# Performance work log

Measured on AMD Instinct MI355X. Metric: run time of the kernel, lower is better.

The kernel has to match this reference:

```python
import jax, jax.numpy as jnp
import numpy as np

B, F, S, H1, H2 = 4096, 512, 32, 64, 32


def setup_inputs() -> dict:
    key = jax.random.key(0)
    ks = jax.random.split(key, 9)
    x = jax.random.normal(ks[0], (B, F), dtype=jnp.float32)
    # ExU layer init: truncated_normal(mean=4, std=0.5) on weight, std=0.5 on bias
    W0 = 4.0 + 0.5 * jax.random.normal(ks[1], (F, S, S), dtype=jnp.float32)
    b0 = 0.5 * jax.random.normal(ks[2], (F, S), dtype=jnp.float32)
    # ReLU hidden layers: xavier-ish weights, small biases
    W1 = jax.random.normal(ks[3], (F, S, H1), dtype=jnp.float32) * np.sqrt(2.0 / (S + H1))
    b1 = 0.5 * jax.random.normal(ks[4], (F, S), dtype=jnp.float32)
    W2 = jax.random.normal(ks[5], (F, H1, H2), dtype=jnp.float32) * np.sqrt(2.0 / (H1 + H2))
    b2 = 0.5 * jax.random.normal(ks[6], (F, H1), dtype=jnp.float32)
    Wl = jax.random.normal(ks[7], (F, H2), dtype=jnp.float32) * np.sqrt(2.0 / (H2 + 1))
    out_bias = jnp.zeros((1,), dtype=jnp.float32)
    return {"x": x, "W0": W0, "b0": b0, "W1": W1, "b1": b1,
            "W2": W2, "b2": b2, "Wl": Wl, "out_bias": out_bias}


def reference(x, W0, b0, W1, b1, W2, b2, Wl, out_bias):
    # ExU shallow layer per feature: clip((x_f - b0_f) @ exp(W0_f), 0, 1)
    # x[:, :, None] - b0 broadcasts scalar feature to (B, F, S)
    h = jnp.clip(jnp.einsum('bfs,fsh->bfh', x[:, :, None] - b0[None], jnp.exp(W0)), 0.0, 1.0)
    # ReLU hidden layers: relu((h - b) @ W)
    h = jax.nn.relu(jnp.einsum('bfs,fsh->bfh', h - b1[None], W1))   # (B, F, H1)
    h = jax.nn.relu(jnp.einsum('bfh,fho->bfo', h - b2[None], W2))   # (B, F, H2)
    # per-feature Linear(H2 -> 1, no bias), concatenated over features
    f_out = jnp.einsum('bfo,fo->bf', h, Wl)                          # (B, F)
    # forward_type == 'sum' (feature_dropout is identity at inference)
    return f_out.sum(axis=-1) + out_bias[0], f_out
```

## Files before the change

kernel.cpp:

```cpp
#include <hip/hip_runtime.h>

typedef __attribute__((ext_vector_type(8))) short short8;
typedef __attribute__((ext_vector_type(4))) float f32x4;
typedef unsigned int uint32;

namespace {
constexpr int F = 512, NB = 4096;
constexpr int RB = 512;
constexpr int FPB = 4;
constexpr int NFQ = F / FPB;
constexpr size_t OFF_W1F  = 0;
constexpr size_t OFF_W2F  = OFF_W1F + (size_t)F * 4 * 64 * 16;
constexpr size_t OFF_TAB  = OFF_W2F + (size_t)F * 4 * 64 * 16;
constexpr size_t OFF_PART = OFF_TAB + (size_t)F * 160 * 4;
constexpr size_t WS_NEED  = OFF_PART + (size_t)NFQ * NB * 4;
}

__device__ __forceinline__ uint32 cvtpk(float lo, float hi) {
    uint32 r;
    asm("v_cvt_pk_bf16_f32 %0, %1, %2" : "=v"(r) : "v"(lo), "v"(hi));
    return r;
}
__device__ __forceinline__ float clip01(float v) {
    return __builtin_amdgcn_fmed3f(v, 0.f, 1.f);
}

__global__ __launch_bounds__(256) void nam_prep(
    const float* __restrict__ W0, const float* __restrict__ b0,
    const float* __restrict__ W1, const float* __restrict__ b1,
    const float* __restrict__ W2, const float* __restrict__ b2,
    char* __restrict__ ws)
{
    const int f = blockIdx.x;
    const int t = threadIdx.x;
    const int lane = t & 63, w = t >> 6, g = lane >> 4, rr = lane & 15;

    __shared__ float LW[2048];
    __shared__ float red[256], red2[256];

    const float* W0f = W0 + (size_t)f * 1024;
    const float* W1f = W1 + (size_t)f * 2048;
    const float* W2f = W2 + (size_t)f * 2048;
    float* tab = (float*)(ws + OFF_TAB) + (size_t)f * 160;
    union U8 { uint32 u[4]; short8 s8; };

    *(float4*)&LW[t * 4] = *(const float4*)&W0f[t * 4];
    __syncthreads();
    {
        int j = t & 31, sc = t >> 5;
        float a = 0.f, c = 0.f;
#pragma unroll
        for (int k = 0; k < 4; ++k) {
            int s = sc * 4 + k;
            float e = expf(LW[s * 32 + j]);
            a += e; c += b0[f * 32 + s] * e;
        }
        red[sc * 32 + j] = a; red2[sc * 32 + j] = c;
    }
    __syncthreads();
    if (t < 32) {
        float a = 0.f, c = 0.f;
#pragma unroll
        for (int k = 0; k < 8; ++k) { a += red[k * 32 + t]; c += red2[k * 32 + t]; }
        tab[t] = a; tab[32 + t] = -c;
    }
    __syncthreads();

    *(float4*)&LW[t * 4]        = *(const float4*)&W1f[t * 4];
    *(float4*)&LW[1024 + t * 4] = *(const float4*)&W1f[1024 + t * 4];
    __syncthreads();
    {
        int j = t & 63, sc = t >> 6;
        float d = 0.f;
#pragma unroll
        for (int k = 0; k < 8; ++k) {
            int s = sc * 8 + k;
            d += b1[f * 32 + s] * LW[s * 64 + j];
        }
        red[sc * 64 + j] = d;
    }
    {
        int mi = w;
        int col = 32 * (mi & 1) + 8 * (rr >> 2) + 4 * (mi >> 1) + (rr & 3);
        int base = (8 * g) * 64 + col;
        U8 v;
        v.u[0] = cvtpk(LW[base],       LW[base + 64]);
        v.u[1] = cvtpk(LW[base + 128], LW[base + 192]);
        v.u[2] = cvtpk(LW[base + 256], LW[base + 320]);
        v.u[3] = cvtpk(LW[base + 384], LW[base + 448]);
        ((short8*)(ws + OFF_W1F))[((size_t)f * 4 + mi) * 64 + lane] = v.s8;
    }
    __syncthreads();
    if (t < 64) {
        float d = red[t] + red[64 + t] + red[128 + t] + red[192 + t];
        int dst = 32 * ((t >> 2) & 1) + 16 * (t >> 5) + 4 * ((t >> 3) & 3) + (t & 3);
        tab[64 + dst] = -d;
    }
    __syncthreads();

    *(float4*)&LW[t * 4]        = *(const float4*)&W2f[t * 4];
    *(float4*)&LW[1024 + t * 4] = *(const float4*)&W2f[1024 + t * 4];
    __syncthreads();
    {
        int o = t & 31, hc = t >> 5;
        float d = 0.f;
#pragma unroll
        for (int k = 0; k < 8; ++k) {
            int h = hc * 8 + k;
            d += b2[f * 64 + h] * LW[h * 32 + o];
        }
        red[hc * 32 + o] = d;
    }
    {
        int m2 = w >> 1, kc = w & 1;
        int base = (32 * kc + 8 * g) * 32 + 16 * m2 + rr;
        U8 v;
        v.u[0] = cvtpk(LW[base],       LW[base + 32]);
        v.u[1] = cvtpk(LW[base + 64],  LW[base + 96]);
        v.u[2] = cvtpk(LW[base + 128], LW[base + 160]);
        v.u[3] = cvtpk(LW[base + 192], LW[base + 224]);
        ((short8*)(ws + OFF_W2F))[((size_t)f * 4 + m2 * 2 + kc) * 64 + lane] = v.s8;
    }
    __syncthreads();
    if (t < 32) {
        float d = 0.f;
#pragma unroll
        for (int k = 0; k < 8; ++k) d += red[k * 32 + t];
        tab[128 + t] = -d;
    }
}

__device__ __forceinline__ void tile_compute(
    float xv, const short8* w1f, const short8 (&w2f)[2][2],
    const f32x4& A0, const f32x4& A1, const f32x4& C0, const f32x4& C1,
    const f32x4* nd1, const f32x4* nd2, f32x4& c0, f32x4& c1)
{
    union U8 { uint32 u[4]; short8 s8; };
    U8 hb;
    hb.u[0] = cvtpk(clip01(fmaf(xv, A0[0], C0[0])), clip01(fmaf(xv, A0[1], C0[1])));
    hb.u[1] = cvtpk(clip01(fmaf(xv, A0[2], C0[2])), clip01(fmaf(xv, A0[3], C0[3])));
    hb.u[2] = cvtpk(clip01(fmaf(xv, A1[0], C1[0])), clip01(fmaf(xv, A1[1], C1[1])));
    hb.u[3] = cvtpk(clip01(fmaf(xv, A1[2], C1[2])), clip01(fmaf(xv, A1[3], C1[3])));
    short8 b0f = hb.s8;

    f32x4 a0 = __builtin_amdgcn_mfma_f32_16x16x32_bf16(w1f[0], b0f, nd1[0], 0, 0, 0);
    f32x4 a1 = __builtin_amdgcn_mfma_f32_16x16x32_bf16(w1f[1], b0f, nd1[1], 0, 0, 0);
    f32x4 a2 = __builtin_amdgcn_mfma_f32_16x16x32_bf16(w1f[2], b0f, nd1[2], 0, 0, 0);
    f32x4 a3 = __builtin_amdgcn_mfma_f32_16x16x32_bf16(w1f[3], b0f, nd1[3], 0, 0, 0);

    U8 r0, r1;
    r0.u[0] = cvtpk(fmaxf(a0[0], 0.f), fmaxf(a0[1], 0.f));
    r0.u[1] = cvtpk(fmaxf(a0[2], 0.f), fmaxf(a0[3], 0.f));
    r0.u[2] = cvtpk(fmaxf(a2[0], 0.f), fmaxf(a2[1], 0.f));
    r0.u[3] = cvtpk(fmaxf(a2[2], 0.f), fmaxf(a2[3], 0.f));
    r1.u[0] = cvtpk(fmaxf(a1[0], 0.f), fmaxf(a1[1], 0.f));
    r1.u[1] = cvtpk(fmaxf(a1[2], 0.f), fmaxf(a1[3], 0.f));
    r1.u[2] = cvtpk(fmaxf(a3[0], 0.f), fmaxf(a3[1], 0.f));
    r1.u[3] = cvtpk(fmaxf(a3[2], 0.f), fmaxf(a3[3], 0.f));

    c0 = __builtin_amdgcn_mfma_f32_16x16x32_bf16(w2f[0][0], r0.s8, nd2[0], 0, 0, 0);
    c0 = __builtin_amdgcn_mfma_f32_16x16x32_bf16(w2f[0][1], r1.s8, c0, 0, 0, 0);
    c1 = __builtin_amdgcn_mfma_f32_16x16x32_bf16(w2f[1][0], r0.s8, nd2[1], 0, 0, 0);
    c1 = __builtin_amdgcn_mfma_f32_16x16x32_bf16(w2f[1][1], r1.s8, c1, 0, 0, 0);
}

__global__ __launch_bounds__(256, 3) void nam_main(
    const float* __restrict__ x, const float* __restrict__ Wl,
    const char* __restrict__ ws, float* __restrict__ fout, float* __restrict__ part)
{
    const int fq = blockIdx.y;
    const int f0 = fq * FPB;
    const int rbase = blockIdx.x * RB;
    const int t = threadIdx.x;
    const int w = t >> 6, lane = t & 63;
    const int g = lane >> 4, rr = lane & 15;
    const int f = f0 + w;

    __shared__ float sx[FPB * RB];
    __shared__ float sfo[FPB * RB];

    {
        float4 v0 = *(const float4*)(x + (size_t)(rbase + t) * F + f0);
        float4 v1 = *(const float4*)(x + (size_t)(rbase + t + 256) * F + f0);
        sx[0 * RB + t] = v0.x; sx[1 * RB + t] = v0.y;
        sx[2 * RB + t] = v0.z; sx[3 * RB + t] = v0.w;
        sx[0 * RB + t + 256] = v1.x; sx[1 * RB + t + 256] = v1.y;
        sx[2 * RB + t + 256] = v1.z; sx[3 * RB + t + 256] = v1.w;
    }

    const short8* w1img = (const short8*)(ws + OFF_W1F);
    const short8* w2img = (const short8*)(ws + OFF_W2F);
    short8 w1f[4], w2f[2][2];
#pragma unroll
    for (int mi = 0; mi < 4; ++mi) w1f[mi] = w1img[((size_t)f * 4 + mi) * 64 + lane];
#pragma unroll
    for (int m2 = 0; m2 < 2; ++m2)
#pragma unroll
        for (int kc = 0; kc < 2; ++kc)
            w2f[m2][kc] = w2img[((size_t)f * 4 + m2 * 2 + kc) * 64 + lane];

    const f32x4* tabv = (const f32x4*)((const float*)(ws + OFF_TAB) + (size_t)f * 160);
    f32x4 A0 = tabv[2 * g], A1 = tabv[2 * g + 1];
    f32x4 C0 = tabv[8 + 2 * g], C1 = tabv[8 + 2 * g + 1];
    f32x4 nd1[4];
#pragma unroll
    for (int mi = 0; mi < 4; ++mi) nd1[mi] = tabv[16 + 4 * mi + g];
    f32x4 nd2[2];
#pragma unroll
    for (int m2 = 0; m2 < 2; ++m2) nd2[m2] = tabv[32 + 4 * m2 + g];
    f32x4 wl0 = *(const f32x4*)(Wl + f * 32 + 4 * g);
    f32x4 wl1 = *(const f32x4*)(Wl + f * 32 + 16 + 4 * g);

    __syncthreads();

    const float* sxf = sx + w * RB;
    float* sfof = sfo + w * RB;

    for (int k = 0; k < 16; ++k) {
        float xv0 = sxf[32 * k + rr];
        float xv1 = sxf[32 * k + 16 + rr];
        f32x4 c00, c01, c10, c11;
        tile_compute(xv0, w1f, w2f, A0, A1, C0, C1, nd1, nd2, c00, c01);
        tile_compute(xv1, w1f, w2f, A0, A1, C0, C1, nd1, nd2, c10, c11);

        float p0 = 0.f, p1 = 0.f;
#pragma unroll
        for (int r = 0; r < 4; ++r) {
            p0 = fmaf(fmaxf(c00[r], 0.f), wl0[r], p0);
            p0 = fmaf(fmaxf(c01[r], 0.f), wl1[r], p0);
            p1 = fmaf(fmaxf(c10[r], 0.f), wl0[r], p1);
            p1 = fmaf(fmaxf(c11[r], 0.f), wl1[r], p1);
        }
        p0 += __shfl_xor(p0, 16, 64);
        p0 += __shfl_xor(p0, 32, 64);
        p1 += __shfl_xor(p1, 16, 64);
        p1 += __shfl_xor(p1, 32, 64);
        if (lane < 16) {
            sfof[32 * k + lane] = p0;
            sfof[32 * k + 16 + lane] = p1;
        }
    }

    __syncthreads();

#pragma unroll
    for (int kk = 0; kk < 2; ++kk) {
        int r = t + 256 * kk;
        float v0 = sfo[0 * RB + r], v1 = sfo[1 * RB + r];
        float v2 = sfo[2 * RB + r], v3 = sfo[3 * RB + r];
        *(float4*)(fout + (size_t)(rbase + r) * F + f0) = make_float4(v0, v1, v2, v3);
        part[(size_t)fq * NB + rbase + r] = (v0 + v1) + (v2 + v3);
    }
}

__global__ __launch_bounds__(256) void nam_sum(const float* __restrict__ part,
                                               const float* __restrict__ ob,
                                               float* __restrict__ out0) {
    int r = blockIdx.x * 256 + threadIdx.x;
    float s = ob[0];
#pragma unroll 8
    for (int q = 0; q < NFQ; ++q) s += part[(size_t)q * NB + r];
    out0[r] = s;
}

namespace fbk { constexpr int S = 32, H1 = 64, H2 = 32, BLK = 256, ROWS = 2, P1 = 36; }
__global__ __launch_bounds__(256, 2) void fb_main(
    const float* __restrict__ x,  const float* __restrict__ W0,
    const float* __restrict__ b0, const float* __restrict__ W1,
    const float* __restrict__ b1, const float* __restrict__ W2,
    const float* __restrict__ b2, const float* __restrict__ Wl,
    float* __restrict__ fout) {
    using namespace fbk;
    const int f = blockIdx.y;
    const int bbase = blockIdx.x * (BLK * ROWS);
    const int t = threadIdx.x;
    __shared__ float W0e[S * S];
    __shared__ float W1t[H1 * P1];
    __shared__ float W2l[H1 * H2];
    __shared__ float sb0[S], sb1[S], sb2[H1];
    __shared__ float sA[S], sC[S], sd1[H1], sd2[H2], sWl[H2];
    {
        float4 wv = *reinterpret_cast<const float4*>(W0 + (size_t)f * S * S + t * 4);
        W0e[t * 4 + 0] = expf(wv.x); W0e[t * 4 + 1] = expf(wv.y);
        W0e[t * 4 + 2] = expf(wv.z); W0e[t * 4 + 3] = expf(wv.w);
    }
    if (t < S) sb0[t] = b0[f * S + t];
    else if (t < 2 * S) sb1[t - S] = b1[f * S + (t - S)];
    else if (t < 2 * S + H1) sb2[t - 2 * S] = b2[f * H1 + (t - 2 * S)];
    else if (t < 2 * S + H1 + H2) sWl[t - 2 * S - H1] = Wl[f * H2 + (t - 2 * S - H1)];
#pragma unroll
    for (int k = 0; k < (S * H1) / BLK; ++k) {
        int i = t + BLK * k; int s = i >> 6, j = i & 63;
        W1t[j * P1 + s] = W1[(size_t)f * S * H1 + i];
    }
#pragma unroll
    for (int k = 0; k < (H1 * H2) / BLK; ++k) {
        int i = t + BLK * k; W2l[i] = W2[(size_t)f * H1 * H2 + i];
    }
    __syncthreads();
    if (t < S) {
        int j = t; float a = 0.f, c = 0.f;
#pragma unroll
        for (int s = 0; s < S; ++s) { float e = W0e[s * S + j]; a += e; c += sb0[s] * e; }
        sA[j] = a; sC[j] = c;
    } else if (t >= 64 && t < 64 + H1) {
        int j = t - 64; float d = 0.f;
#pragma unroll
        for (int s = 0; s < S; ++s) d += sb1[s] * W1t[j * P1 + s];
        sd1[j] = d;
    } else if (t >= 128 && t < 128 + H2) {
        int o = t - 128; float d = 0.f;
#pragma unroll
        for (int h = 0; h < H1; ++h) d += sb2[h] * W2l[h * H2 + o];
        sd2[o] = d;
    }
    __syncthreads();
    const int ra = bbase + t, rb = bbase + BLK + t;
    const float xa = x[(size_t)ra * F + f], xb = x[(size_t)rb * F + f];
    float h0a[S], h0b[S];
#pragma unroll
    for (int j = 0; j < S; ++j) {
        float A = sA[j], C = sC[j];
        h0a[j] = fminf(fmaxf(fmaf(xa, A, -C), 0.f), 1.f);
        h0b[j] = fminf(fmaxf(fmaf(xb, A, -C), 0.f), 1.f);
    }
    float acc2a[H2], acc2b[H2];
#pragma unroll
    for (int o = 0; o < H2; ++o) { float d = sd2[o]; acc2a[o] = -d; acc2b[o] = -d; }
#pragma unroll 2
    for (int j = 0; j < H1; ++j) {
        float wr[S];
#pragma unroll
        for (int q = 0; q < S / 4; ++q)
            *reinterpret_cast<float4*>(&wr[4 * q]) = reinterpret_cast<const float4*>(&W1t[j * P1])[q];
        float d1j = sd1[j];
        float pa0 = -d1j, pa1 = 0.f, pb0 = -d1j, pb1 = 0.f;
#pragma unroll
        for (int s = 0; s < S; s += 2) {
            pa0 = fmaf(h0a[s], wr[s], pa0); pb0 = fmaf(h0b[s], wr[s], pb0);
            pa1 = fmaf(h0a[s + 1], wr[s + 1], pa1); pb1 = fmaf(h0b[s + 1], wr[s + 1], pb1);
        }
        float h1a = fmaxf(pa0 + pa1, 0.f), h1b = fmaxf(pb0 + pb1, 0.f);
        float w2r[H2];
#pragma unroll
        for (int q = 0; q < H2 / 4; ++q)
            *reinterpret_cast<float4*>(&w2r[4 * q]) = reinterpret_cast<const float4*>(&W2l[j * H2])[q];
#pragma unroll
        for (int o = 0; o < H2; ++o) {
            acc2a[o] = fmaf(h1a, w2r[o], acc2a[o]); acc2b[o] = fmaf(h1b, w2r[o], acc2b[o]);
        }
    }
    float outa = 0.f, outb = 0.f;
#pragma unroll
    for (int o = 0; o < H2; ++o) {
        outa = fmaf(fmaxf(acc2a[o], 0.f), sWl[o], outa);
        outb = fmaf(fmaxf(acc2b[o], 0.f), sWl[o], outb);
    }
    fout[(size_t)ra * F + f] = outa;
    fout[(size_t)rb * F + f] = outb;
}
__global__ __launch_bounds__(256) void fb_rowsum(
    const float* __restrict__ fout, const float* __restrict__ out_bias,
    float* __restrict__ out0) {
    const int wave = threadIdx.x >> 6, lane = threadIdx.x & 63;
    const int b = blockIdx.x * 4 + wave;
    float s = 0.f;
#pragma unroll
    for (int k = 0; k < F / 64; ++k) s += fout[(size_t)b * F + k * 64 + lane];
#pragma unroll
    for (int off = 32; off; off >>= 1) s += __shfl_down(s, off, 64);
    if (lane == 0) out0[b] = s + out_bias[0];
}

extern "C" void kernel_launch(void* const* d_in, const int* in_sizes, int n_in,
                              void* d_out, int out_size, void* d_ws, size_t ws_size,
                              hipStream_t stream) {
    const float* x  = (const float*)d_in[0];
    const float* W0 = (const float*)d_in[1];
    const float* b0 = (const float*)d_in[2];
    const float* W1 = (const float*)d_in[3];
    const float* b1 = (const float*)d_in[4];
    const float* W2 = (const float*)d_in[5];
    const float* b2 = (const float*)d_in[6];
    const float* Wl = (const float*)d_in[7];
    const float* ob = (const float*)d_in[8];

    float* out0 = (float*)d_out;
    float* fout = out0 + NB;

    if (ws_size >= WS_NEED) {
        char* ws = (char*)d_ws;
        float* part = (float*)(ws + OFF_PART);
        nam_prep<<<F, 256, 0, stream>>>(W0, b0, W1, b1, W2, b2, ws);
        nam_main<<<dim3(NB / RB, NFQ), 256, 0, stream>>>(x, Wl, ws, fout, part);
        nam_sum <<<NB / 256, 256, 0, stream>>>(part, ob, out0);
    } else {
        dim3 grid(NB / (fbk::BLK * fbk::ROWS), F);
        fb_main<<<grid, fbk::BLK, 0, stream>>>(x, W0, b0, W1, b1, W2, b2, Wl, fout);
        fb_rowsum<<<NB / 4, 256, 0, stream>>>(fout, ob, out0);
    }
}
```

Before: 48.90 us.

## Halve row block, process one tile per iteration, reduce partials through LDS

Halves the rows per block to 256 and raises the launch-bounds occupancy hint from 3 to 4 blocks per CU, doubling the grid. The inner loop now handles one 16-row tile per iteration instead of two. The cross-lane shuffle reduction is replaced by storing per-group partials to a shared buffer and summing them with vector LDS reads, and the x staging buffer is reused to hold per-feature outputs. The aim is lower register pressure and fewer shuffles. The cost is less ILP per wave, more LDS traffic, and weights reloaded by twice as many blocks.

```diff
diff --git a/kernel.cpp b/kernel.cpp
--- a/kernel.cpp
+++ b/kernel.cpp
@@ -6,7 +6,7 @@
 
 namespace {
 constexpr int F = 512, NB = 4096;
-constexpr int RB = 512;
+constexpr int RB = 256;
 constexpr int FPB = 4;
 constexpr int NFQ = F / FPB;
 constexpr size_t OFF_W1F  = 0;
@@ -130,41 +130,25 @@
     }
 }
 
-__device__ __forceinline__ void tile_compute(
-    float xv, const short8* w1f, const short8 (&w2f)[2][2],
-    const f32x4& A0, const f32x4& A1, const f32x4& C0, const f32x4& C1,
-    const f32x4* nd1, const f32x4* nd2, f32x4& c0, f32x4& c1)
-{
-    union U8 { uint32 u[4]; short8 s8; };
-    U8 hb;
+__device__ __forceinline__ short8 make_hb(float xv, const f32x4& A0, const f32x4& A1,
+                                          const f32x4& C0, const f32x4& C1) {
+    union { uint32 u[4]; short8 s8; } hb;
     hb.u[0] = cvtpk(clip01(fmaf(xv, A0[0], C0[0])), clip01(fmaf(xv, A0[1], C0[1])));
     hb.u[1] = cvtpk(clip01(fmaf(xv, A0[2], C0[2])), clip01(fmaf(xv, A0[3], C0[3])));
     hb.u[2] = cvtpk(clip01(fmaf(xv, A1[0], C1[0])), clip01(fmaf(xv, A1[1], C1[1])));
     hb.u[3] = cvtpk(clip01(fmaf(xv, A1[2], C1[2])), clip01(fmaf(xv, A1[3], C1[3])));
-    short8 b0f = hb.s8;
-
-    f32x4 a0 = __builtin_amdgcn_mfma_f32_16x16x32_bf16(w1f[0], b0f, nd1[0], 0, 0, 0);
-    f32x4 a1 = __builtin_amdgcn_mfma_f32_16x16x32_bf16(w1f[1], b0f, nd1[1], 0, 0, 0);
-    f32x4 a2 = __builtin_amdgcn_mfma_f32_16x16x32_bf16(w1f[2], b0f, nd1[2], 0, 0, 0);
-    f32x4 a3 = __builtin_amdgcn_mfma_f32_16x16x32_bf16(w1f[3], b0f, nd1[3], 0, 0, 0);
-
-    U8 r0, r1;
-    r0.u[0] = cvtpk(fmaxf(a0[0], 0.f), fmaxf(a0[1], 0.f));
-    r0.u[1] = cvtpk(fmaxf(a0[2], 0.f), fmaxf(a0[3], 0.f));
-    r0.u[2] = cvtpk(fmaxf(a2[0], 0.f), fmaxf(a2[1], 0.f));
-    r0.u[3] = cvtpk(fmaxf(a2[2], 0.f), fmaxf(a2[3], 0.f));
-    r1.u[0] = cvtpk(fmaxf(a1[0], 0.f), fmaxf(a1[1], 0.f));
-    r1.u[1] = cvtpk(fmaxf(a1[2], 0.f), fmaxf(a1[3], 0.f));
-    r1.u[2] = cvtpk(fmaxf(a3[0], 0.f), fmaxf(a3[1], 0.f));
-    r1.u[3] = cvtpk(fmaxf(a3[2], 0.f), fmaxf(a3[3], 0.f));
-
-    c0 = __builtin_amdgcn_mfma_f32_16x16x32_bf16(w2f[0][0], r0.s8, nd2[0], 0, 0, 0);
-    c0 = __builtin_amdgcn_mfma_f32_16x16x32_bf16(w2f[0][1], r1.s8, c0, 0, 0, 0);
-    c1 = __builtin_amdgcn_mfma_f32_16x16x32_bf16(w2f[1][0], r0.s8, nd2[1], 0, 0, 0);
-    c1 = __builtin_amdgcn_mfma_f32_16x16x32_bf16(w2f[1][1], r1.s8, c1, 0, 0, 0);
-}
-
-__global__ __launch_bounds__(256, 3) void nam_main(
+    return hb.s8;
+}
+__device__ __forceinline__ short8 packrelu(const f32x4& x, const f32x4& y) {
+    union { uint32 u[4]; short8 s8; } r;
+    r.u[0] = cvtpk(fmaxf(x[0], 0.f), fmaxf(x[1], 0.f));
+    r.u[1] = cvtpk(fmaxf(x[2], 0.f), fmaxf(x[3], 0.f));
+    r.u[2] = cvtpk(fmaxf(y[0], 0.f), fmaxf(y[1], 0.f));
+    r.u[3] = cvtpk(fmaxf(y[2], 0.f), fmaxf(y[3], 0.f));
+    return r.s8;
+}
+
+__global__ __launch_bounds__(256, 4) void nam_main(
     const float* __restrict__ x, const float* __restrict__ Wl,
     const char* __restrict__ ws, float* __restrict__ fout, float* __restrict__ part)
 {
@@ -177,15 +161,12 @@
     const int f = f0 + w;
 
     __shared__ float sx[FPB * RB];
-    __shared__ float sfo[FPB * RB];
-
-    {
-        float4 v0 = *(const float4*)(x + (size_t)(rbase + t) * F + f0);
-        float4 v1 = *(const float4*)(x + (size_t)(rbase + t + 256) * F + f0);
-        sx[0 * RB + t] = v0.x; sx[1 * RB + t] = v0.y;
-        sx[2 * RB + t] = v0.z; sx[3 * RB + t] = v0.w;
-        sx[0 * RB + t + 256] = v1.x; sx[1 * RB + t + 256] = v1.y;
-        sx[2 * RB + t + 256] = v1.z; sx[3 * RB + t + 256] = v1.w;
+    __shared__ float psum[FPB * RB * 4];
+
+    {
+        float4 v = *(const float4*)(x + (size_t)(rbase + t) * F + f0);
+        sx[0 * RB + t] = v.x; sx[1 * RB + t] = v.y;
+        sx[2 * RB + t] = v.z; sx[3 * RB + t] = v.w;
     }
 
     const short8* w1img = (const short8*)(ws + OFF_W1F);
@@ -214,40 +195,47 @@
     __syncthreads();
 
     const float* sxf = sx + w * RB;
-    float* sfof = sfo + w * RB;
+    float* psw = psum + w * (RB * 4);
 
     for (int k = 0; k < 16; ++k) {
-        float xv0 = sxf[32 * k + rr];
-        float xv1 = sxf[32 * k + 16 + rr];
-        f32x4 c00, c01, c10, c11;
-        tile_compute(xv0, w1f, w2f, A0, A1, C0, C1, nd1, nd2, c00, c01);
-        tile_compute(xv1, w1f, w2f, A0, A1, C0, C1, nd1, nd2, c10, c11);
-
-        float p0 = 0.f, p1 = 0.f;
+        float xv = sxf[16 * k + rr];
+        short8 hb = make_hb(xv, A0, A1, C0, C1);
+
+        f32x4 a0 = __builtin_amdgcn_mfma_f32_16x16x32_bf16(w1f[0], hb, nd1[0], 0, 0, 0);
+        f32x4 a1 = __builtin_amdgcn_mfma_f32_16x16x32_bf16(w1f[1], hb, nd1[1], 0, 0, 0);
+        f32x4 a2 = __builtin_amdgcn_mfma_f32_16x16x32_bf16(w1f[2], hb, nd1[2], 0, 0, 0);
+        f32x4 a3 = __builtin_amdgcn_mfma_f32_16x16x32_bf16(w1f[3], hb, nd1[3], 0, 0, 0);
+
+        short8 r0 = packrelu(a0, a2);
+        short8 r1 = packrelu(a1, a3);
+
+        f32x4 c0 = __builtin_amdgcn_mfma_f32_16x16x32_bf16(w2f[0][0], r0, nd2[0], 0, 0, 0);
+        c0 = __builtin_amdgcn_mfma_f32_16x16x32_bf16(w2f[0][1], r1, c0, 0, 0, 0);
+        f32x4 c1 = __builtin_amdgcn_mfma_f32_16x16x32_bf16(w2f[1][0], r0, nd2[1], 0, 0, 0);
+        c1 = __builtin_amdgcn_mfma_f32_16x16x32_bf16(w2f[1][1], r1, c1, 0, 0, 0);
+
+        float p = 0.f;
 #pragma unroll
         for (int r = 0; r < 4; ++r) {
-            p0 = fmaf(fmaxf(c00[r], 0.f), wl0[r], p0);
-            p0 = fmaf(fmaxf(c01[r], 0.f), wl1[r], p0);
-            p1 = fmaf(fmaxf(c10[r], 0.f), wl0[r], p1);
-            p1 = fmaf(fmaxf(c11[r], 0.f), wl1[r], p1);
-        }
-        p0 += __shfl_xor(p0, 16, 64);
-        p0 += __shfl_xor(p0, 32, 64);
-        p1 += __shfl_xor(p1, 16, 64);
-        p1 += __shfl_xor(p1, 32, 64);
-        if (lane < 16) {
-            sfof[32 * k + lane] = p0;
-            sfof[32 * k + 16 + lane] = p1;
-        }
-    }
-
-    __syncthreads();
-
-#pragma unroll
-    for (int kk = 0; kk < 2; ++kk) {
-        int r = t + 256 * kk;
-        float v0 = sfo[0 * RB + r], v1 = sfo[1 * RB + r];
-        float v2 = sfo[2 * RB + r], v3 = sfo[3 * RB + r];
+            p = fmaf(fmaxf(c0[r], 0.f), wl0[r], p);
+            p = fmaf(fmaxf(c1[r], 0.f), wl1[r], p);
+        }
+        psw[(16 * k + rr) * 4 + g] = p;
+    }
+
+#pragma unroll
+    for (int i = 0; i < 4; ++i) {
+        int row = i * 64 + lane;
+        f32x4 v = *(const f32x4*)&psw[row * 4];
+        ((float*)sx)[w * RB + row] = (v[0] + v[1]) + (v[2] + v[3]);
+    }
+
+    __syncthreads();
+
+    {
+        int r = t;
+        float v0 = sx[0 * RB + r], v1 = sx[1 * RB + r];
+        float v2 = sx[2 * RB + r], v3 = sx[3 * RB + r];
         *(float4*)(fout + (size_t)(rbase + r) * F + f0) = make_float4(v0, v1, v2, v3);
         part[(size_t)fq * NB + rbase + r] = (v0 + v1) + (v2 + v3);
     }
```

New measurement: 44.95 us, median of 3. 8.1% less time.
